# Kernel tuning notes

Hardware: AMD Instinct MI355X
Metric: run time of the kernel (lower is better)

Reference implementation:

```python
import jax, jax.numpy as jnp
import numpy as np

B, H, W, C = 2, 64, 128, 256
HEADS, K, HIDDEN = 8, 9, 1024
HD = C // HEADS
EPS = 1e-5


def _ln(z, g, b):
    m = z.mean(-1, keepdims=True)
    v = ((z - m) ** 2).mean(-1, keepdims=True)
    return (z - m) / jnp.sqrt(v + EPS) * g + b


def _bilinear(img, coords):
    # img: [hd, H, W]; coords: [H, W, K, 2] in [-1, 1] (x=width, y=height), align_corners=True
    Hh, Ww = img.shape[1], img.shape[2]
    cx = (coords[..., 0] + 1.0) * 0.5 * (Ww - 1)
    cy = (coords[..., 1] + 1.0) * 0.5 * (Hh - 1)
    x0 = jnp.floor(cx); y0 = jnp.floor(cy)
    wx = cx - x0; wy = cy - y0
    x0i = jnp.clip(x0, 0, Ww - 1).astype(jnp.int32)
    x1i = jnp.clip(x0 + 1, 0, Ww - 1).astype(jnp.int32)
    y0i = jnp.clip(y0, 0, Hh - 1).astype(jnp.int32)
    y1i = jnp.clip(y0 + 1, 0, Hh - 1).astype(jnp.int32)
    g = lambda yi, xi: img[:, yi, xi]  # [hd, H, W, K]
    return (g(y0i, x0i) * (1 - wy) * (1 - wx) + g(y0i, x1i) * (1 - wy) * wx
            + g(y1i, x0i) * wy * (1 - wx) + g(y1i, x1i) * wy * wx)


def setup_inputs() -> dict:
    key = jax.random.key(0)
    ks = jax.random.split(key, 12)
    s = 0.02
    return {
        "x": jax.random.normal(ks[0], (B, H * W, C), jnp.float32),
        "ref_point": jax.random.uniform(ks[1], (1, H, W, K, 2), jnp.float32, -1.0, 1.0),
        "ln1_g": jnp.ones((C,), jnp.float32), "ln1_b": jnp.zeros((C,), jnp.float32),
        "w_v": jax.random.normal(ks[2], (C, C), jnp.float32) * s, "b_v": jnp.zeros((C,), jnp.float32),
        "w_off": jax.random.normal(ks[3], (C, HEADS * K * 2), jnp.float32) * s, "b_off": jnp.zeros((HEADS * K * 2,), jnp.float32),
        "w_attn": jax.random.normal(ks[4], (C, HEADS * K), jnp.float32) * s, "b_attn": jnp.zeros((HEADS * K,), jnp.float32),
        "w_out": jax.random.normal(ks[5], (C, C), jnp.float32) * s, "b_out": jnp.zeros((C,), jnp.float32),
        "ln2_g": jnp.ones((C,), jnp.float32), "ln2_b": jnp.zeros((C,), jnp.float32),
        "w1": jax.random.normal(ks[6], (C, HIDDEN), jnp.float32) * s, "b1": jnp.zeros((HIDDEN,), jnp.float32),
        "w_dw": jax.random.normal(ks[7], (HIDDEN, 1, 3, 3), jnp.float32) * s, "b_dw": jnp.zeros((HIDDEN,), jnp.float32),
        "w2": jax.random.normal(ks[8], (HIDDEN, C), jnp.float32) * s, "b2": jnp.zeros((C,), jnp.float32),
    }


def reference(x, ref_point, ln1_g, ln1_b, w_v, b_v, w_off, b_off, w_attn, b_attn,
              w_out, b_out, ln2_g, ln2_b, w1, b1, w_dw, b_dw, w2, b2):
    # --- Sphere deformable self-attention branch ---
    xn = _ln(x, ln1_g, ln1_b).reshape(B, H, W, C)
    v = (xn @ w_v + b_v).reshape(B, H, W, HEADS, HD)
    v = jnp.transpose(v, (0, 3, 4, 1, 2))                               # [B, heads, hd, H, W]
    off = (xn @ w_off + b_off).reshape(B, H, W, HEADS, K, 2)
    locs = ref_point[:, :, :, None, :, :] + off                          # [B, H, W, heads, K, 2]
    locs = jnp.transpose(locs, (0, 3, 1, 2, 4, 5))                       # [B, heads, H, W, K, 2]
    attn = jax.nn.softmax((xn @ w_attn + b_attn).reshape(B, H, W, HEADS, K), axis=-1)
    sampled = jax.vmap(jax.vmap(_bilinear))(v, locs)                     # [B, heads, hd, H, W, K]
    agg = jnp.einsum('bndhwk,bhwnk->bhwnd', sampled, attn).reshape(B, H, W, C)
    x = x + ((agg @ w_out) + b_out).reshape(B, H * W, C)
    # --- LeFF branch: linear -> GELU -> circular-pad depthwise conv -> GELU -> linear ---
    y = _ln(x, ln2_g, ln2_b)
    h = jax.nn.gelu(y @ w1 + b1, approximate=False).reshape(B, H, W, HIDDEN)
    h = jnp.transpose(h, (0, 3, 1, 2))                                   # NCHW
    h = jnp.pad(h, ((0, 0), (0, 0), (0, 0), (1, 1)), mode='wrap')        # circular pad along width
    h = jnp.pad(h, ((0, 0), (0, 0), (1, 1), (0, 0)))                     # zero pad along height
    h = jax.lax.conv_general_dilated(h, w_dw, (1, 1), 'VALID',
                                     feature_group_count=HIDDEN,
                                     dimension_numbers=('NCHW', 'OIHW', 'NCHW'))
    h = jax.nn.gelu(h + b_dw[None, :, None, None], approximate=False)
    h = jnp.transpose(h, (0, 2, 3, 1)).reshape(B, H * W, HIDDEN)
    return x + h @ w2 + b2
```

## Files before the change

kernel.cpp:

```cpp
#include <hip/hip_runtime.h>
#include <hip/hip_bf16.h>
#include <hip/hip_fp8.h>
#include <type_traits>

constexpr int Bc = 2, Hc = 64, Wc = 128, Cc = 256;
constexpr int HEADS = 8, KPT = 9, HIDDEN = 1024;
constexpr int HD = Cc / HEADS;
constexpr int NPIX = Hc * Wc;
constexpr int Mrows = Bc * NPIX;
constexpr int NQKV = 512;

typedef __attribute__((ext_vector_type(4))) float f32x4;
typedef __attribute__((ext_vector_type(8))) short bf16x8;

__device__ __forceinline__ float bf2f(unsigned short u) {
    union { unsigned int i; float f; } c; c.i = ((unsigned int)u) << 16; return c.f;
}
__device__ __forceinline__ unsigned short f2bf(float f) {
    __hip_bfloat16 h = __float2bfloat16(f);
    return *reinterpret_cast<unsigned short*>(&h);
}
__device__ __forceinline__ unsigned char f2fp8(float f) {
    return __hip_fp8_e4m3(f).__x;
}
__device__ __forceinline__ float fp82f(unsigned char u) {
    __hip_fp8_e4m3 v; v.__x = u; return (float)v;
}
__device__ __forceinline__ float gelu_exact(float x) {
    return 0.5f * x * (1.0f + erff(x * 0.70710678118654752f));
}
__device__ __forceinline__ void gl2lds16(const void* g, void* l) {
    __builtin_amdgcn_global_load_lds(
        (const __attribute__((address_space(1))) unsigned int*)g,
        (__attribute__((address_space(3))) unsigned int*)l, 16, 0, 0);
}

__global__ __launch_bounds__(256) void prepln_kernel(
        const float* __restrict__ x, const float* __restrict__ ln1_g,
        const float* __restrict__ ln1_b, unsigned short* __restrict__ xn,
        const float* __restrict__ w_v, const float* __restrict__ b_v,
        const float* __restrict__ w_off, const float* __restrict__ b_off,
        const float* __restrict__ w_attn, const float* __restrict__ b_attn,
        const float* __restrict__ w_out, const float* __restrict__ w1,
        const float* __restrict__ w2, const float* __restrict__ w_dw,
        unsigned short* __restrict__ qkvT, float* __restrict__ qkvB,
        unsigned short* __restrict__ woutT, unsigned short* __restrict__ w1T,
        unsigned short* __restrict__ w2T, float* __restrict__ wdwT) {
    const int t = threadIdx.x;
    if (blockIdx.x < Mrows / 4) {
        const int r = blockIdx.x * 4 + (t >> 6);
        const int l = t & 63;
        const size_t base = (size_t)r * Cc + l * 4;
        const float4 v = *reinterpret_cast<const float4*>(x + base);
        float s  = v.x + v.y + v.z + v.w;
        float s2 = v.x * v.x + v.y * v.y + v.z * v.z + v.w * v.w;
        #pragma unroll
        for (int o = 32; o > 0; o >>= 1) { s += __shfl_down(s, o); s2 += __shfl_down(s2, o); }
        s = __shfl(s, 0); s2 = __shfl(s2, 0);
        const float mean = s * (1.0f / Cc);
        const float rstd = rsqrtf(s2 * (1.0f / Cc) - mean * mean + 1e-5f);
        const float4 gv = *reinterpret_cast<const float4*>(ln1_g + l * 4);
        const float4 bv = *reinterpret_cast<const float4*>(ln1_b + l * 4);
        ushort4 o;
        o.x = f2bf((v.x - mean) * rstd * gv.x + bv.x);
        o.y = f2bf((v.y - mean) * rstd * gv.y + bv.y);
        o.z = f2bf((v.z - mean) * rstd * gv.z + bv.z);
        o.w = f2bf((v.w - mean) * rstd * gv.w + bv.w);
        *reinterpret_cast<ushort4*>(xn + base) = o;
        return;
    }
    const int blk = blockIdx.x - Mrows / 4;
    if (blk < NQKV) {
        const int n = blk;
        float val = 0.0f;
        if (n < 256)       val = w_v[t * 256 + n];
        else if (n < 400)  val = w_off[t * 144 + (n - 256)];
        else if (n < 472)  val = w_attn[t * 72 + (n - 400)];
        qkvT[n * 256 + t] = f2bf(val);
        if (t == 0) {
            float bv = 0.0f;
            if (n < 256)      bv = b_v[n];
            else if (n < 400) bv = b_off[n - 256];
            else if (n < 472) bv = b_attn[n - 400];
            qkvB[n] = bv;
        }
    } else if (blk < NQKV + 256) {
        const int n = blk - NQKV;
        woutT[n * 256 + t] = f2bf(w_out[t * 256 + n]);
    } else if (blk < NQKV + 256 + 1024) {
        const int n = blk - (NQKV + 256);
        w1T[n * 256 + t] = f2bf(w1[t * 1024 + n]);
    } else if (blk < NQKV + 256 + 1024 + 256) {
        const int n = blk - (NQKV + 256 + 1024);
        #pragma unroll
        for (int k = t; k < 1024; k += 256)
            w2T[n * 1024 + k] = f2bf(w2[k * 256 + n]);
    } else {
        const int j = blk - (NQKV + 256 + 1024 + 256);
        #pragma unroll
        for (int c = t; c < HIDDEN; c += 256)
            wdwT[j * HIDDEN + c] = w_dw[c * 9 + j];
    }
}

template<int BN, bool GELU, bool RESID, typename TO>
__global__ __launch_bounds__(512) void mfma_gemm(
        const unsigned short* __restrict__ A,
        const unsigned short* __restrict__ BT,
        const float* __restrict__ bias,
        const float* __restrict__ resid,
        TO* __restrict__ Out,
        int N, int K) {
    constexpr int WCOLS = (BN == 128) ? 4 : 2;
    constexpr int WROWS = 8 / WCOLS;
    constexpr int MI = 128 / (WROWS * 16);
    constexpr int NI = BN / (WCOLS * 16);
    constexpr int ACH = 2;
    constexpr int BCH = (BN / 8) / 8;
    constexpr int LA = ACH + BCH;
    constexpr int BUFB = 16384 + BN * 128;
    __shared__ __align__(16) char lds[2 * BUFB];
    const int t = threadIdx.x;
    const int w = t >> 6;
    const int l = t & 63;
    const int row0 = blockIdx.x * 128;
    const int col0 = blockIdx.y * BN;
    const int wr = (w / WCOLS) * (MI * 16);
    const int wc = (w % WCOLS) * (NI * 16);

    const int srow = l >> 3;
    const int selem = ((l & 7) ^ srow) * 8;

    auto stage = [&](char* buf, int k0) {
        unsigned short* As_ = (unsigned short*)buf;
        unsigned short* Bs_ = (unsigned short*)(buf + 16384);
        #pragma unroll
        for (int i = 0; i < ACH; ++i) {
            const int c = w + i * 8;
            const int row = c * 8 + srow;
            gl2lds16(A + (size_t)(row0 + row) * K + k0 + selem, As_ + c * 512);
        }
        #pragma unroll
        for (int i = 0; i < BCH; ++i) {
            const int c = w + i * 8;
            const int row = c * 8 + srow;
            gl2lds16(BT + (size_t)(col0 + row) * K + k0 + selem, Bs_ + c * 512);
        }
    };

    f32x4 acc[MI][NI] = {};
    const int nt = K / 64;

    stage(lds, 0);
    stage(lds + BUFB, 64);

    for (int tt = 0; tt < nt; ++tt) {
        if (tt + 1 < nt) {
            if constexpr (LA == 4) asm volatile("s_waitcnt vmcnt(4)" ::: "memory");
            else                   asm volatile("s_waitcnt vmcnt(3)" ::: "memory");
        } else {
            asm volatile("s_waitcnt vmcnt(0)" ::: "memory");
        }
        __builtin_amdgcn_s_barrier();
        __builtin_amdgcn_sched_barrier(0);

        const char* Ab = lds + (size_t)(tt & 1) * BUFB;
        const char* Bb = Ab + 16384;
        #pragma unroll
        for (int ks = 0; ks < 2; ++ks) {
            const int kb = ks * 64 + (l >> 4) * 16;
            bf16x8 af[MI], bfr[NI];
            #pragma unroll
            for (int mi = 0; mi < MI; ++mi) {
                const int row = wr + mi * 16 + (l & 15);
                af[mi] = *(const bf16x8*)(Ab + row * 128 + (kb ^ ((row & 7) << 4)));
            }
            #pragma unroll
            for (int ni = 0; ni < NI; ++ni) {
                const int row = wc + ni * 16 + (l & 15);
                bfr[ni] = *(const bf16x8*)(Bb + row * 128 + (kb ^ ((row & 7) << 4)));
            }
            #pragma unroll
            for (int mi = 0; mi < MI; ++mi)
                #pragma unroll
                for (int ni = 0; ni < NI; ++ni)
                    acc[mi][ni] = __builtin_amdgcn_mfma_f32_16x16x32_bf16(
                        af[mi], bfr[ni], acc[mi][ni], 0, 0, 0);
        }
        __builtin_amdgcn_s_barrier();
        __builtin_amdgcn_sched_barrier(0);
        if (tt + 2 < nt) stage(lds + (size_t)(tt & 1) * BUFB, (tt + 2) * 64);
    }

    constexpr int ROWB = BN * (int)sizeof(TO);
    const int lrow = (l >> 4) * 4;
    const int lcol = l & 15;
    #pragma unroll
    for (int ni = 0; ni < NI; ++ni) {
        const int col = wc + ni * 16 + lcol;
        const float bb = bias[col0 + col];
        #pragma unroll
        for (int mi = 0; mi < MI; ++mi) {
            #pragma unroll
            for (int r = 0; r < 4; ++r) {
                const int row = wr + mi * 16 + lrow + r;
                float v = acc[mi][ni][r] + bb;
                if constexpr (GELU) v = gelu_exact(v);
                if constexpr (std::is_same<TO, unsigned short>::value) {
                    *(unsigned short*)(lds + row * ROWB + ((col * 2) ^ ((row & 7) << 4))) = f2bf(v);
                } else if constexpr (std::is_same<TO, unsigned char>::value) {
                    *(unsigned char*)(lds + row * ROWB + ((col) ^ ((row & 7) << 4))) = f2fp8(v);
                } else {
                    *(float*)(lds + row * ROWB + ((col * 4) ^ ((row & 7) << 4))) = v;
                }
            }
        }
    }
    __syncthreads();
    constexpr int CPR = ROWB / 16;
    constexpr int RPI = 512 / CPR;
    const int ck = t % CPR;
    #pragma unroll
    for (int it = 0; it < 128 / RPI; ++it) {
        const int row = (t / CPR) + it * RPI;
        const int bo = ck * 16;
        const char* src = lds + row * ROWB + (bo ^ ((row & 7) << 4));
        if constexpr (std::is_same<TO, unsigned short>::value) {
            *(int4*)(Out + (size_t)(row0 + row) * N + col0 + bo / 2) = *(const int4*)src;
        } else if constexpr (std::is_same<TO, unsigned char>::value) {
            *(int4*)(Out + (size_t)(row0 + row) * N + col0 + bo) = *(const int4*)src;
        } else {
            float4 val = *(const float4*)src;
            if constexpr (RESID) {
                const float4 rv = *(const float4*)(resid + (size_t)(row0 + row) * N + col0 + bo / 4);
                val.x += rv.x; val.y += rv.y; val.z += rv.z; val.w += rv.w;
            }
            *(float4*)((float*)Out + (size_t)(row0 + row) * N + col0 + bo / 4) = val;
        }
    }
}

__global__ __launch_bounds__(512) void wout_ln2_kernel(
        const unsigned short* __restrict__ A,
        const unsigned short* __restrict__ BT,
        const float* __restrict__ bias,
        const float* __restrict__ resid,
        const float* __restrict__ g2, const float* __restrict__ b2,
        float* __restrict__ Out,
        unsigned short* __restrict__ Y) {
    constexpr int BM = 64, K = 256;
    constexpr int ABYTES = BM * 128;
    constexpr int BUFB = ABYTES + 256 * 128;
    __shared__ __align__(16) char lds[2 * BUFB];
    const int t = threadIdx.x;
    const int w = t >> 6;
    const int l = t & 63;
    const int row0 = blockIdx.x * BM;
    const int wr = (w >> 2) * 32;
    const int wc = (w & 3) * 64;

    const int srow = l >> 3;
    const int selem = ((l & 7) ^ srow) * 8;

    auto stage = [&](char* buf, int k0) {
        unsigned short* As_ = (unsigned short*)buf;
        unsigned short* Bs_ = (unsigned short*)(buf + ABYTES);
        {
            const int row = w * 8 + srow;
            gl2lds16(A + (size_t)(row0 + row) * K + k0 + selem, As_ + w * 512);
        }
        #pragma unroll
        for (int i = 0; i < 4; ++i) {
            const int c = w + i * 8;
            const int row = c * 8 + srow;
            gl2lds16(BT + (size_t)row * K + k0 + selem, Bs_ + c * 512);
        }
    };

    f32x4 acc[2][4] = {};
    stage(lds, 0);
    stage(lds + BUFB, 64);

    for (int tt = 0; tt < 4; ++tt) {
        if (tt + 1 < 4) asm volatile("s_waitcnt vmcnt(5)" ::: "memory");
        else            asm volatile("s_waitcnt vmcnt(0)" ::: "memory");
        __builtin_amdgcn_s_barrier();
        __builtin_amdgcn_sched_barrier(0);

        const char* Ab = lds + (size_t)(tt & 1) * BUFB;
        const char* Bb = Ab + ABYTES;
        #pragma unroll
        for (int ks = 0; ks < 2; ++ks) {
            const int kb = ks * 64 + (l >> 4) * 16;
            bf16x8 af[2], bfr[4];
            #pragma unroll
            for (int mi = 0; mi < 2; ++mi) {
                const int row = wr + mi * 16 + (l & 15);
                af[mi] = *(const bf16x8*)(Ab + row * 128 + (kb ^ ((row & 7) << 4)));
            }
            #pragma unroll
            for (int ni = 0; ni < 4; ++ni) {
                const int row = wc + ni * 16 + (l & 15);
                bfr[ni] = *(const bf16x8*)(Bb + row * 128 + (kb ^ ((row & 7) << 4)));
            }
            #pragma unroll
            for (int mi = 0; mi < 2; ++mi)
                #pragma unroll
                for (int ni = 0; ni < 4; ++ni)
                    acc[mi][ni] = __builtin_amdgcn_mfma_f32_16x16x32_bf16(
                        af[mi], bfr[ni], acc[mi][ni], 0, 0, 0);
        }
        __builtin_amdgcn_s_barrier();
        __builtin_amdgcn_sched_barrier(0);
        if (tt + 2 < 4) stage(lds + (size_t)(tt & 1) * BUFB, (tt + 2) * 64);
    }

    const int lrow = (l >> 4) * 4;
    const int lcol = l & 15;
    #pragma unroll
    for (int ni = 0; ni < 4; ++ni) {
        const int col = wc + ni * 16 + lcol;
        const float bb = bias[col];
        #pragma unroll
        for (int mi = 0; mi < 2; ++mi) {
            #pragma unroll
            for (int r = 0; r < 4; ++r) {
                const int row = wr + mi * 16 + lrow + r;
                *(float*)(lds + row * 1024 + ((col * 4) ^ ((row & 7) << 4))) = acc[mi][ni][r] + bb;
            }
        }
    }
    __syncthreads();
    const float4 gv = *reinterpret_cast<const float4*>(g2 + l * 4);
    const float4 bv = *reinterpret_cast<const float4*>(b2 + l * 4);
    #pragma unroll
    for (int it = 0; it < 8; ++it) {
        const int r = w + it * 8;
        float4 v = *(const float4*)(lds + r * 1024 + ((l * 16) ^ ((r & 7) << 4)));
        const float4 rv = *(const float4*)(resid + (size_t)(row0 + r) * Cc + l * 4);
        v.x += rv.x; v.y += rv.y; v.z += rv.z; v.w += rv.w;
        float s  = v.x + v.y + v.z + v.w;
        float s2 = v.x * v.x + v.y * v.y + v.z * v.z + v.w * v.w;
        #pragma unroll
        for (int o = 32; o > 0; o >>= 1) { s += __shfl_down(s, o); s2 += __shfl_down(s2, o); }
        s = __shfl(s, 0); s2 = __shfl(s2, 0);
        const float mean = s * (1.0f / Cc);
        const float rstd = rsqrtf(s2 * (1.0f / Cc) - mean * mean + 1e-5f);
        *(float4*)(Out + (size_t)(row0 + r) * Cc + l * 4) = v;
        ushort4 o;
        o.x = f2bf((v.x - mean) * rstd * gv.x + bv.x);
        o.y = f2bf((v.y - mean) * rstd * gv.y + bv.y);
        o.z = f2bf((v.z - mean) * rstd * gv.z + bv.z);
        o.w = f2bf((v.w - mean) * rstd * gv.w + bv.w);
        *(ushort4*)(Y + (size_t)(row0 + r) * Cc + l * 4) = o;
    }
}

__global__ __launch_bounds__(256) void sample_kernel(const unsigned short* __restrict__ F,
        const float* __restrict__ refp, unsigned short* __restrict__ agg) {
    constexpr int PPB = 4;
    constexpr int nblk = Mrows / PPB;
    const int bid = blockIdx.x;
    const int qi = (bid & 7) * (nblk / 8) + (bid >> 3);
    const int m0 = qi * PPB;
    const int b = m0 / NPIX;
    const int pix0 = m0 - b * NPIX;
    const int t = threadIdx.x;
    __shared__ int4   s_idx[PPB][72];
    __shared__ float4 s_w[PPB][72];
    __shared__ float  s_lg[PPB][72];

    for (int idx = t; idx < PPB * 72; idx += 256) {
        const int p = idx / 72, hk = idx - p * 72;
        const int head = hk / 9, k = hk - head * 9;
        const int m = m0 + p, pix = pix0 + p;
        const size_t fb = (size_t)m * NQKV;
        const unsigned int ou = *(const unsigned int*)(F + fb + 256 + head * 18 + k * 2);
        const float ox = __uint_as_float(ou << 16);
        const float oy = __uint_as_float(ou & 0xffff0000u);
        const float2 rr = *(const float2*)(refp + ((size_t)pix * KPT + k) * 2);
        const float cx = (rr.x + ox + 1.0f) * 0.5f * (Wc - 1);
        const float cy = (rr.y + oy + 1.0f) * 0.5f * (Hc - 1);
        const float fx = floorf(cx), fy = floorf(cy);
        const float wx = cx - fx, wy = cy - fy;
        const int x0 = min(max((int)fx, 0), Wc - 1);
        const int x1 = min(max((int)fx + 1, 0), Wc - 1);
        const int y0 = min(max((int)fy, 0), Hc - 1);
        const int y1 = min(max((int)fy + 1, 0), Hc - 1);
        s_idx[p][hk] = make_int4(y0 * Wc + x0, y0 * Wc + x1, y1 * Wc + x0, y1 * Wc + x1);
        s_w[p][hk] = make_float4((1.0f - wy) * (1.0f - wx), (1.0f - wy) * wx,
                                 wy * (1.0f - wx), wy * wx);
        s_lg[p][hk] = bf2f(F[fb + 400 + hk]);
    }
    __syncthreads();
    for (int idx = t; idx < PPB * 72; idx += 256) {
        const int p = idx / 72, hk = idx - p * 72;
        const int h9 = (hk / 9) * 9;
        float mx = -1e30f;
        #pragma unroll
        for (int k = 0; k < 9; ++k) mx = fmaxf(mx, s_lg[p][h9 + k]);
        float sm = 0.0f;
        #pragma unroll
        for (int k = 0; k < 9; ++k) sm += __expf(s_lg[p][h9 + k] - mx);
        const float a = __expf(s_lg[p][hk] - mx) / sm;
        float4 w = s_w[p][hk];
        w.x *= a; w.y *= a; w.z *= a; w.w *= a;
        s_w[p][hk] = w;
    }
    __syncthreads();
    const int p = t >> 6, tl = t & 63;
    const int head = tl >> 3, dq = tl & 7;
    const unsigned short* vb = F + (size_t)b * NPIX * NQKV + head * HD + dq * 4;
    float a0 = 0.f, a1 = 0.f, a2 = 0.f, a3 = 0.f;
    #pragma unroll
    for (int k = 0; k < 9; ++k) {
        const int hk = head * 9 + k;
        const int4   ix = s_idx[p][hk];
        const float4 ww = s_w[p][hk];
        {
            const uint2 u = *(const uint2*)(vb + (size_t)ix.x * NQKV);
            a0 += __uint_as_float(u.x << 16) * ww.x;
            a1 += __uint_as_float(u.x & 0xffff0000u) * ww.x;
            a2 += __uint_as_float(u.y << 16) * ww.x;
            a3 += __uint_as_float(u.y & 0xffff0000u) * ww.x;
        }
        {
            const uint2 u = *(const uint2*)(vb + (size_t)ix.y * NQKV);
            a0 += __uint_as_float(u.x << 16) * ww.y;
            a1 += __uint_as_float(u.x & 0xffff0000u) * ww.y;
            a2 += __uint_as_float(u.y << 16) * ww.y;
            a3 += __uint_as_float(u.y & 0xffff0000u) * ww.y;
        }
        {
            const uint2 u = *(const uint2*)(vb + (size_t)ix.z * NQKV);
            a0 += __uint_as_float(u.x << 16) * ww.z;
            a1 += __uint_as_float(u.x & 0xffff0000u) * ww.z;
            a2 += __uint_as_float(u.y << 16) * ww.z;
            a3 += __uint_as_float(u.y & 0xffff0000u) * ww.z;
        }
        {
            const uint2 u = *(const uint2*)(vb + (size_t)ix.w * NQKV);
            a0 += __uint_as_float(u.x << 16) * ww.w;
            a1 += __uint_as_float(u.x & 0xffff0000u) * ww.w;
            a2 += __uint_as_float(u.y << 16) * ww.w;
            a3 += __uint_as_float(u.y & 0xffff0000u) * ww.w;
        }
    }
    ushort4 o;
    o.x = f2bf(a0); o.y = f2bf(a1); o.z = f2bf(a2); o.w = f2bf(a3);
    *reinterpret_cast<ushort4*>(agg + (size_t)(m0 + p) * Cc + tl * 4) = o;
}

__global__ __launch_bounds__(256) void dwconv_kernel(const unsigned char* __restrict__ h,
        const float* __restrict__ wdwT, const float* __restrict__ bdw,
        unsigned short* __restrict__ h2) {
    constexpr int NQ = 8;
    constexpr int nblk = Mrows / NQ;
    const int bid = blockIdx.x;
    const int qi = (bid & 7) * (nblk / 8) + (bid >> 3);
    const int m0 = qi * NQ;
    const int b = m0 / NPIX;
    const int pix0 = m0 - b * NPIX;
    const int y = pix0 / Wc, x0 = pix0 - y * Wc;
    const int t = threadIdx.x;
    const int c0 = t * 4;

    float wreg[9][4];
    #pragma unroll
    for (int j = 0; j < 9; ++j) {
        const float4 wv = *reinterpret_cast<const float4*>(wdwT + j * HIDDEN + c0);
        wreg[j][0] = wv.x; wreg[j][1] = wv.y; wreg[j][2] = wv.z; wreg[j][3] = wv.w;
    }

    float acc[NQ][4] = {};
    #pragma unroll
    for (int dy = -1; dy <= 1; ++dy) {
        const int yy = y + dy;
        if (yy < 0 || yy >= Hc) continue;
        const size_t rowbase = ((size_t)b * NPIX + (size_t)yy * Wc) * HIDDEN + c0;
        #pragma unroll
        for (int j = 0; j < NQ + 2; ++j) {
            const int xx = (x0 + j - 1 + Wc) & (Wc - 1);
            const uchar4 hv = *reinterpret_cast<const uchar4*>(h + rowbase + (size_t)xx * HIDDEN);
            const float f0 = fp82f(hv.x), f1 = fp82f(hv.y), f2 = fp82f(hv.z), f3 = fp82f(hv.w);
            #pragma unroll
            for (int q = 0; q < NQ; ++q) {
                if (q >= j - 2 && q <= j) {
                    const int wj = (dy + 1) * 3 + (j - q);
                    acc[q][0] += f0 * wreg[wj][0];
                    acc[q][1] += f1 * wreg[wj][1];
                    acc[q][2] += f2 * wreg[wj][2];
                    acc[q][3] += f3 * wreg[wj][3];
                }
            }
        }
    }
    const float4 bb = *reinterpret_cast<const float4*>(bdw + c0);
    #pragma unroll
    for (int q = 0; q < NQ; ++q) {
        ushort4 o;
        o.x = f2bf(gelu_exact(acc[q][0] + bb.x));
        o.y = f2bf(gelu_exact(acc[q][1] + bb.y));
        o.z = f2bf(gelu_exact(acc[q][2] + bb.z));
        o.w = f2bf(gelu_exact(acc[q][3] + bb.w));
        *reinterpret_cast<ushort4*>(h2 + (size_t)(m0 + q) * HIDDEN + c0) = o;
    }
}

extern "C" void kernel_launch(void* const* d_in, const int* in_sizes, int n_in,
                              void* d_out, int out_size, void* d_ws, size_t ws_size,
                              hipStream_t stream) {
    const float* x      = (const float*)d_in[0];
    const float* refp   = (const float*)d_in[1];
    const float* ln1_g  = (const float*)d_in[2];
    const float* ln1_b  = (const float*)d_in[3];
    const float* w_v    = (const float*)d_in[4];
    const float* b_v    = (const float*)d_in[5];
    const float* w_off  = (const float*)d_in[6];
    const float* b_off  = (const float*)d_in[7];
    const float* w_attn = (const float*)d_in[8];
    const float* b_attn = (const float*)d_in[9];
    const float* w_out  = (const float*)d_in[10];
    const float* b_out  = (const float*)d_in[11];
    const float* ln2_g  = (const float*)d_in[12];
    const float* ln2_b  = (const float*)d_in[13];
    const float* w1     = (const float*)d_in[14];
    const float* b1     = (const float*)d_in[15];
    const float* w_dw   = (const float*)d_in[16];
    const float* b_dw   = (const float*)d_in[17];
    const float* w2     = (const float*)d_in[18];
    const float* b2     = (const float*)d_in[19];
    float* out = (float*)d_out;

    char* wsb = (char*)d_ws;
    unsigned short* Abuf = (unsigned short*)(wsb);
    unsigned short* F    = (unsigned short*)(wsb + (8ull  << 20));
    unsigned short* ybuf = (unsigned short*)(wsb + (8ull  << 20));
    unsigned char*  hbuf = (unsigned char*)(wsb + (32ull << 20));
    unsigned short* h2   = (unsigned short*)(wsb);
    size_t woff = 64ull << 20;
    unsigned short* qkvT = (unsigned short*)(wsb + woff); woff += (size_t)NQKV * 256 * 2;
    unsigned short* woutT= (unsigned short*)(wsb + woff); woff += 256 * 256 * 2;
    unsigned short* w1T  = (unsigned short*)(wsb + woff); woff += 1024 * 256 * 2;
    unsigned short* w2T  = (unsigned short*)(wsb + woff); woff += 256 * 1024 * 2;
    float*          wdwT = (float*)(wsb + woff);          woff += 9 * 1024 * 4;
    float*          qkvB = (float*)(wsb + woff);

    prepln_kernel<<<Mrows / 4 + NQKV + 256 + 1024 + 256 + 9, 256, 0, stream>>>(
        x, ln1_g, ln1_b, Abuf,
        w_v, b_v, w_off, b_off, w_attn, b_attn, w_out, w1, w2, w_dw,
        qkvT, qkvB, woutT, w1T, w2T, wdwT);
    mfma_gemm<128, false, false, unsigned short><<<dim3(Mrows / 128, NQKV / 128), 512, 0, stream>>>(
        Abuf, qkvT, qkvB, nullptr, F, NQKV, 256);
    sample_kernel<<<Mrows / 4, 256, 0, stream>>>(F, refp, Abuf);
    wout_ln2_kernel<<<Mrows / 64, 512, 0, stream>>>(
        Abuf, woutT, b_out, x, ln2_g, ln2_b, out, ybuf);
    mfma_gemm<128, true, false, unsigned char><<<dim3(Mrows / 128, 1024 / 128), 512, 0, stream>>>(
        ybuf, w1T, b1, nullptr, hbuf, 1024, 256);
    dwconv_kernel<<<Mrows / 8, 256, 0, stream>>>(hbuf, wdwT, b_dw, h2);
    mfma_gemm<64, false, true, float><<<dim3(Mrows / 128, 256 / 64), 512, 0, stream>>>(
        h2, w2T, b2, out, out, 256, 1024);
}
```

Baseline: 124.2 us.

## Quantize the final w2 GEMM to FP8 with scaled weights and a dedicated kernel

```diff
diff --git a/kernel.cpp b/kernel.cpp
--- a/kernel.cpp
+++ b/kernel.cpp
@@ -45,7 +45,7 @@
         const float* __restrict__ w2, const float* __restrict__ w_dw,
         unsigned short* __restrict__ qkvT, float* __restrict__ qkvB,
         unsigned short* __restrict__ woutT, unsigned short* __restrict__ w1T,
-        unsigned short* __restrict__ w2T, float* __restrict__ wdwT) {
+        unsigned char* __restrict__ w2T8, float* __restrict__ wdwT) {
     const int t = threadIdx.x;
     if (blockIdx.x < Mrows / 4) {
         const int r = blockIdx.x * 4 + (t >> 6);
@@ -94,7 +94,7 @@
         const int n = blk - (NQKV + 256 + 1024);
         #pragma unroll
         for (int k = t; k < 1024; k += 256)
-            w2T[n * 1024 + k] = f2bf(w2[k * 256 + n]);
+            w2T8[n * 1024 + k] = f2fp8(w2[k * 256 + n] * 32.0f);
     } else {
         const int j = blk - (NQKV + 256 + 1024 + 256);
         #pragma unroll
@@ -240,6 +240,111 @@
     }
 }
 
+__global__ __launch_bounds__(512) void w2_gemm_fp8(
+        const unsigned char* __restrict__ A,
+        const unsigned char* __restrict__ BT,
+        const float* __restrict__ bias,
+        const float* __restrict__ resid,
+        float* __restrict__ Out,
+        int N, int K) {
+    constexpr int ABYTES = 128 * 128;
+    constexpr int BUFB = ABYTES + 64 * 128;
+    __shared__ __align__(16) char lds[2 * BUFB];
+    const int t = threadIdx.x;
+    const int w = t >> 6;
+    const int l = t & 63;
+    const int row0 = blockIdx.x * 128;
+    const int col0 = blockIdx.y * 64;
+    const int wr = (w >> 1) * 32;
+    const int wc = (w & 1) * 32;
+
+    const int srow = l >> 3;
+    const int sbyte = ((l & 7) ^ srow) * 16;
+
+    auto stage = [&](char* buf, int k0) {
+        unsigned char* As_ = (unsigned char*)buf;
+        unsigned char* Bs_ = (unsigned char*)(buf + ABYTES);
+        #pragma unroll
+        for (int i = 0; i < 2; ++i) {
+            const int c = w + i * 8;
+            const int row = c * 8 + srow;
+            gl2lds16(A + (size_t)(row0 + row) * K + k0 + sbyte, As_ + c * 1024);
+        }
+        {
+            const int row = w * 8 + srow;
+            gl2lds16(BT + (size_t)(col0 + row) * K + k0 + sbyte, Bs_ + w * 1024);
+        }
+    };
+
+    f32x4 acc[2][2] = {};
+    const int nt = K / 128;
+
+    stage(lds, 0);
+    stage(lds + BUFB, 128);
+
+    for (int tt = 0; tt < nt; ++tt) {
+        if (tt + 1 < nt) asm volatile("s_waitcnt vmcnt(3)" ::: "memory");
+        else             asm volatile("s_waitcnt vmcnt(0)" ::: "memory");
+        __builtin_amdgcn_s_barrier();
+        __builtin_amdgcn_sched_barrier(0);
+
+        const char* Ab = lds + (size_t)(tt & 1) * BUFB;
+        const char* Bb = Ab + ABYTES;
+        #pragma unroll
+        for (int ks = 0; ks < 4; ++ks) {
+            const int kb = ks * 32 + (l >> 4) * 8;
+            long af[2], bfr[2];
+            #pragma unroll
+            for (int mi = 0; mi < 2; ++mi) {
+                const int row = wr + mi * 16 + (l & 15);
+                af[mi] = *(const long*)(Ab + row * 128 + (kb ^ ((row & 7) << 4)));
+            }
+            #pragma unroll
+            for (int ni = 0; ni < 2; ++ni) {
+                const int row = wc + ni * 16 + (l & 15);
+                bfr[ni] = *(const long*)(Bb + row * 128 + (kb ^ ((row & 7) << 4)));
+            }
+            #pragma unroll
+            for (int mi = 0; mi < 2; ++mi)
+                #pragma unroll
+                for (int ni = 0; ni < 2; ++ni)
+                    acc[mi][ni] = __builtin_amdgcn_mfma_f32_16x16x32_fp8_fp8(
+                        af[mi], bfr[ni], acc[mi][ni], 0, 0, 0);
+        }
+        __builtin_amdgcn_s_barrier();
+        __builtin_amdgcn_sched_barrier(0);
+        if (tt + 2 < nt) stage(lds + (size_t)(tt & 1) * BUFB, (tt + 2) * 128);
+    }
+
+    const int lrow = (l >> 4) * 4;
+    const int lcol = l & 15;
+    #pragma unroll
+    for (int ni = 0; ni < 2; ++ni) {
+        const int col = wc + ni * 16 + lcol;
+        const float bb = bias[col0 + col];
+        #pragma unroll
+        for (int mi = 0; mi < 2; ++mi) {
+            #pragma unroll
+            for (int r = 0; r < 4; ++r) {
+                const int row = wr + mi * 16 + lrow + r;
+                *(float*)(lds + row * 256 + ((col * 4) ^ ((row & 7) << 4)))
+                    = acc[mi][ni][r] * 0.03125f + bb;
+            }
+        }
+    }
+    __syncthreads();
+    const int ck = t & 15;
+    #pragma unroll
+    for (int it = 0; it < 4; ++it) {
+        const int row = (t >> 4) + it * 32;
+        const int bo = ck * 16;
+        float4 val = *(const float4*)(lds + row * 256 + (bo ^ ((row & 7) << 4)));
+        const float4 rv = *(const float4*)(resid + (size_t)(row0 + row) * N + col0 + bo / 4);
+        val.x += rv.x; val.y += rv.y; val.z += rv.z; val.w += rv.w;
+        *(float4*)(Out + (size_t)(row0 + row) * N + col0 + bo / 4) = val;
+    }
+}
+
 __global__ __launch_bounds__(512) void wout_ln2_kernel(
         const unsigned short* __restrict__ A,
         const unsigned short* __restrict__ BT,
@@ -453,7 +558,7 @@
 
 __global__ __launch_bounds__(256) void dwconv_kernel(const unsigned char* __restrict__ h,
         const float* __restrict__ wdwT, const float* __restrict__ bdw,
-        unsigned short* __restrict__ h2) {
+        unsigned char* __restrict__ h2) {
     constexpr int NQ = 8;
     constexpr int nblk = Mrows / NQ;
     const int bid = blockIdx.x;
@@ -498,12 +603,12 @@
     const float4 bb = *reinterpret_cast<const float4*>(bdw + c0);
     #pragma unroll
     for (int q = 0; q < NQ; ++q) {
-        ushort4 o;
-        o.x = f2bf(gelu_exact(acc[q][0] + bb.x));
-        o.y = f2bf(gelu_exact(acc[q][1] + bb.y));
-        o.z = f2bf(gelu_exact(acc[q][2] + bb.z));
-        o.w = f2bf(gelu_exact(acc[q][3] + bb.w));
-        *reinterpret_cast<ushort4*>(h2 + (size_t)(m0 + q) * HIDDEN + c0) = o;
+        uchar4 o;
+        o.x = f2fp8(gelu_exact(acc[q][0] + bb.x));
+        o.y = f2fp8(gelu_exact(acc[q][1] + bb.y));
+        o.z = f2fp8(gelu_exact(acc[q][2] + bb.z));
+        o.w = f2fp8(gelu_exact(acc[q][3] + bb.w));
+        *reinterpret_cast<uchar4*>(h2 + (size_t)(m0 + q) * HIDDEN + c0) = o;
     }
 }
 
@@ -537,19 +642,19 @@
     unsigned short* F    = (unsigned short*)(wsb + (8ull  << 20));
     unsigned short* ybuf = (unsigned short*)(wsb + (8ull  << 20));
     unsigned char*  hbuf = (unsigned char*)(wsb + (32ull << 20));
-    unsigned short* h2   = (unsigned short*)(wsb);
+    unsigned char*  h2   = (unsigned char*)(wsb + (16ull << 20));
     size_t woff = 64ull << 20;
     unsigned short* qkvT = (unsigned short*)(wsb + woff); woff += (size_t)NQKV * 256 * 2;
     unsigned short* woutT= (unsigned short*)(wsb + woff); woff += 256 * 256 * 2;
     unsigned short* w1T  = (unsigned short*)(wsb + woff); woff += 1024 * 256 * 2;
-    unsigned short* w2T  = (unsigned short*)(wsb + woff); woff += 256 * 1024 * 2;
+    unsigned char*  w2T8 = (unsigned char*)(wsb + woff);  woff += 256 * 1024;
     float*          wdwT = (float*)(wsb + woff);          woff += 9 * 1024 * 4;
     float*          qkvB = (float*)(wsb + woff);
 
     prepln_kernel<<<Mrows / 4 + NQKV + 256 + 1024 + 256 + 9, 256, 0, stream>>>(
         x, ln1_g, ln1_b, Abuf,
         w_v, b_v, w_off, b_off, w_attn, b_attn, w_out, w1, w2, w_dw,
-        qkvT, qkvB, woutT, w1T, w2T, wdwT);
+        qkvT, qkvB, woutT, w1T, w2T8, wdwT);
     mfma_gemm<128, false, false, unsigned short><<<dim3(Mrows / 128, NQKV / 128), 512, 0, stream>>>(
         Abuf, qkvT, qkvB, nullptr, F, NQKV, 256);
     sample_kernel<<<Mrows / 4, 256, 0, stream>>>(F, refp, Abuf);
@@ -558,6 +663,6 @@
     mfma_gemm<128, true, false, unsigned char><<<dim3(Mrows / 128, 1024 / 128), 512, 0, stream>>>(
         ybuf, w1T, b1, nullptr, hbuf, 1024, 256);
     dwconv_kernel<<<Mrows / 8, 256, 0, stream>>>(hbuf, wdwT, b_dw, h2);
-    mfma_gemm<64, false, true, float><<<dim3(Mrows / 128, 256 / 64), 512, 0, stream>>>(
-        h2, w2T, b2, out, out, 256, 1024);
-}
+    w2_gemm_fp8<<<dim3(Mrows / 128, 256 / 64), 512, 0, stream>>>(
+        h2, w2T8, b2, out, out, 256, 1024);
+}
```

Measured after the change: 117.5 us. 1.06x faster.
